# Kernel optimization log

Measured on AMD Instinct MI355X. Metric: run time of the kernel, lower is better.

Reference implementation:

```python
import jax, jax.numpy as jnp
import numpy as np

N = 20000      # nodes
E = 320000     # edges (avg degree 16)
S = 2          # extra feature axis (mean-pooled before fc)
IN = 128       # in_feats
H = 246        # n_hidden (must be 246 to match fc = Linear(246, 1))


def setup_inputs() -> dict:
    key = jax.random.key(0)
    ks = jax.random.split(key, 8)
    feat = jax.random.normal(ks[0], (N, S, IN), jnp.float32)
    src = jax.random.randint(ks[1], (E,), 0, N, jnp.int32)
    dst = jax.random.randint(ks[2], (E,), 0, N, jnp.int32)
    glorot = lambda k, shp, fan: jax.random.normal(k, shp, jnp.float32) / np.sqrt(fan).astype(np.float32)
    return {
        "features": feat,
        "src": src,
        "dst": dst,
        "W0": glorot(ks[3], (IN, H), IN), "b0": jnp.zeros((H,), jnp.float32),
        "W1": glorot(ks[4], (H, H), H),   "b1": jnp.zeros((H,), jnp.float32),
        "W2": glorot(ks[5], (H, H), H),   "b2": jnp.zeros((H,), jnp.float32),
        "fc_w": glorot(ks[6], (H, 1), H), "fc_b": jnp.zeros((1,), jnp.float32),
    }


def reference(features, src, dst, W0, b0, W1, b1, W2, b2, fc_w, fc_b):
    # DGL GraphConv, norm='both': h' = act( D_in^{-1/2} A D_out^{-1/2} h W + b )
    ones = jnp.ones((src.shape[0],), jnp.float32)
    out_deg = jax.ops.segment_sum(ones, src, num_segments=N)
    in_deg = jax.ops.segment_sum(ones, dst, num_segments=N)
    norm_out = jax.lax.rsqrt(jnp.maximum(out_deg, 1.0))[:, None, None]  # [N,1,1]
    norm_in = jax.lax.rsqrt(jnp.maximum(in_deg, 1.0))[:, None, None]

    def graph_conv(h, W, b):
        h = h * norm_out                                      # [N,S,F] scale by src-side norm
        agg = jax.ops.segment_sum(h[src], dst, num_segments=N)  # gather->scatter-add over edges
        agg = agg * norm_in
        return jax.nn.relu(agg @ W + b)

    h = graph_conv(features.astype(jnp.float32), W0, b0)
    # dropout between layers is identity in eval mode
    h = graph_conv(h, W1, b1)
    h = graph_conv(h, W2, b2)
    return h.mean(axis=1) @ fc_w + fc_b  # [N,1]
```

## Files before the change

kernel.cpp:

```cpp
#include <hip/hip_runtime.h>
#include <hip/hip_fp16.h>

#define NN 20000
#define NE 320000
#define SS 2
#define FIN 128
#define FH 246
#define MPAD 40064

typedef _Float16 f16x8 __attribute__((ext_vector_type(8)));
typedef float f32x4 __attribute__((ext_vector_type(4)));

__global__ void degree_kernel(const int* __restrict__ src, const int* __restrict__ dst,
                              int* __restrict__ deg_out, int* __restrict__ deg_in) {
    int e = blockIdx.x * blockDim.x + threadIdx.x;
    if (e < NE) {
        atomicAdd(&deg_out[src[e]], 1);
        atomicAdd(&deg_in[dst[e]], 1);
    }
}

__global__ void alloc_kernel(const int* __restrict__ deg_out, const int* __restrict__ deg_in,
                             float* __restrict__ norm_out, float* __restrict__ norm_in,
                             int* __restrict__ row_start, int* __restrict__ cursor,
                             int* __restrict__ counter) {
    __shared__ int smem[256];
    __shared__ int base_s;
    int tid = threadIdx.x;
    int i = blockIdx.x * 256 + tid;
    int v  = (i < NN) ? deg_in[i] : 0;
    int vp = (v + 3) & ~3;
    smem[tid] = vp;
    __syncthreads();
    for (int off = 1; off < 256; off <<= 1) {
        int t = (tid >= off) ? smem[tid - off] : 0;
        __syncthreads();
        smem[tid] += t;
        __syncthreads();
    }
    int incl = smem[tid];
    if (tid == 0) base_s = atomicAdd(counter, smem[255]);
    __syncthreads();
    if (i < NN) {
        int excl = base_s + incl - vp;
        row_start[i] = excl;
        cursor[i]    = excl;
        norm_out[i] = rsqrtf(fmaxf((float)deg_out[i], 1.0f));
        norm_in[i]  = rsqrtf(fmaxf((float)v, 1.0f));
    }
}

__global__ void scatter_kernel(const int* __restrict__ src, const int* __restrict__ dst,
                               int* __restrict__ cursor, ushort* __restrict__ sorted_src) {
    int e = blockIdx.x * blockDim.x + threadIdx.x;
    if (e < NE) {
        int d = dst[e];
        int pos = atomicAdd(&cursor[d], 1);
        sorted_src[pos] = (ushort)src[e];
    }
}

__global__ void pad_fill(const int* __restrict__ row_start, const int* __restrict__ deg_in,
                         ushort* __restrict__ sorted_src) {
    int n = blockIdx.x * 256 + threadIdx.x;
    if (n < NN) {
        int d = deg_in[n];
        int beg = row_start[n] + d;
        int end = row_start[n] + ((d + 3) & ~3);
        for (int p = beg; p < end; ++p) sorted_src[p] = (ushort)NN;
    }
}

__global__ void convert_w_all(const float* __restrict__ W0, const float* __restrict__ W1,
                              const float* __restrict__ W2,
                              ushort* __restrict__ Wh0, ushort* __restrict__ Wl0,
                              ushort* __restrict__ Wh1, ushort* __restrict__ Wl1,
                              ushort* __restrict__ Wh2, ushort* __restrict__ Wl2) {
    int n = blockIdx.x, k = threadIdx.x;
    const float* W; ushort* Wh; ushort* Wl; int K;
    if (blockIdx.y == 0)      { W = W0; Wh = Wh0; Wl = Wl0; K = FIN; }
    else if (blockIdx.y == 1) { W = W1; Wh = Wh1; Wl = Wl1; K = FH; }
    else                      { W = W2; Wh = Wh2; Wl = Wl2; K = FH; }
    float v = (k < K && n < 246) ? W[k * 246 + n] : 0.f;
    _Float16 h = (_Float16)v;
    _Float16 l = (_Float16)(v - (float)h);
    int c16 = n >> 4, lr = n & 15, kt = k >> 5, quad = (k >> 3) & 3, j = k & 7;
    int off = ((c16 * 8 + kt) * 64 + quad * 16 + lr) * 8 + j;
    Wh[off] = *(ushort*)&h;
    Wl[off] = *(ushort*)&l;
}

__global__ void init_out(float* __restrict__ out, const float* __restrict__ fcb,
                         float* __restrict__ norm_out) {
    int i = blockIdx.x * 256 + threadIdx.x;
    if (i < NN) out[i] = fcb[0];
    if (i == 0) norm_out[NN] = 0.f;
}

__global__ void zero_pads(ushort* __restrict__ Ah, ushort* __restrict__ Al) {
    int i = blockIdx.x * 256 + threadIdx.x;
    if (i < 4096) {
        int kt = i >> 9, r = i & 511;
        int m = NN * SS + (r >> 3), j = r & 7;
        size_t o = ((size_t)kt * MPAD + m) * 8 + j;
        ((unsigned long long*)Ah)[o] = 0ull;
        ((unsigned long long*)Al)[o] = 0ull;
    }
}

template<int F4ROW, int NCH, bool NORM>
__global__ void aggregate4(const float* __restrict__ h,
                           const int* __restrict__ row_start,
                           const int* __restrict__ deg_in,
                           const ushort* __restrict__ sorted_src,
                           const float* __restrict__ norm_out,
                           const float* __restrict__ norm_in,
                           ushort* __restrict__ Ah, ushort* __restrict__ Al) {
    constexpr int IHALF = F4ROW / 2;
    int g  = threadIdx.x >> 4;
    int l  = threadIdx.x & 15;
    int cb = blockIdx.x & (NCH - 1);
    int nb = blockIdx.x / NCH;
    int n  = nb * 8 + g;
    if (n >= NN) return;
    int idx = cb * 16 + l;
    const float4* hv = (const float4*)h;
    int beg = row_start[n];
    int end = beg + ((deg_in[n] + 3) & ~3);
    float4 acc = {0.f, 0.f, 0.f, 0.f};
    ushort4 ss;
    if (beg < end) ss = *(const ushort4*)&sorted_src[beg];
    for (int i = beg; i < end; i += 4) {
        ushort4 cur = ss;
        if (i + 4 < end) ss = *(const ushort4*)&sorted_src[i + 4];
        int s0 = cur.x, s1 = cur.y, s2 = cur.z, s3 = cur.w;
        if (NORM) {
            float n0 = norm_out[s0], n1 = norm_out[s1];
            float n2 = norm_out[s2], n3 = norm_out[s3];
            float4 v0 = hv[(size_t)(s0 < NN ? s0 : NN - 1) * F4ROW + idx];
            float4 v1 = hv[(size_t)(s1 < NN ? s1 : NN - 1) * F4ROW + idx];
            float4 v2 = hv[(size_t)(s2 < NN ? s2 : NN - 1) * F4ROW + idx];
            float4 v3 = hv[(size_t)(s3 < NN ? s3 : NN - 1) * F4ROW + idx];
            acc.x += v0.x * n0 + v1.x * n1 + v2.x * n2 + v3.x * n3;
            acc.y += v0.y * n0 + v1.y * n1 + v2.y * n2 + v3.y * n3;
            acc.z += v0.z * n0 + v1.z * n1 + v2.z * n2 + v3.z * n3;
            acc.w += v0.w * n0 + v1.w * n1 + v2.w * n2 + v3.w * n3;
        } else {
            float4 v0 = hv[(size_t)s0 * F4ROW + idx];
            float4 v1 = hv[(size_t)s1 * F4ROW + idx];
            float4 v2 = hv[(size_t)s2 * F4ROW + idx];
            float4 v3 = hv[(size_t)s3 * F4ROW + idx];
            acc.x += v0.x + v1.x + v2.x + v3.x;
            acc.y += v0.y + v1.y + v2.y + v3.y;
            acc.z += v0.z + v1.z + v2.z + v3.z;
            acc.w += v0.w + v1.w + v2.w + v3.w;
        }
    }
    float ni = norm_in[n];
    float v[4] = {acc.x * ni, acc.y * ni, acc.z * ni, acc.w * ni};
    ushort hp[4], lp[4];
#pragma unroll
    for (int j = 0; j < 4; ++j) {
        _Float16 hh = (_Float16)v[j];
        _Float16 ll = (_Float16)(v[j] - (float)hh);
        hp[j] = *(ushort*)&hh;
        lp[j] = *(ushort*)&ll;
    }
    int s  = (idx >= IHALF);
    int ik = idx & (IHALF - 1);
    size_t o = ((size_t)(ik >> 3) * MPAD + n * 2 + s) * 8 + (ik & 7);
    unsigned long long hv64, lv64;
    __builtin_memcpy(&hv64, hp, 8);
    __builtin_memcpy(&lv64, lp, 8);
    __builtin_nontemporal_store(hv64, (unsigned long long*)Ah + o);
    __builtin_nontemporal_store(lv64, (unsigned long long*)Al + o);
}

template<int KP, bool FUSE>
__global__ __launch_bounds__(256, 1) void gemm_breg(const ushort* __restrict__ Ah,
                                                    const ushort* __restrict__ Al,
                                                    const ushort* __restrict__ Whp,
                                                    const ushort* __restrict__ Wlp,
                                                    const float* __restrict__ b,
                                                    void* __restrict__ outv,
                                                    const float* __restrict__ fcw,
                                                    const float* __restrict__ nrm) {
    constexpr int NT = KP / 32;
    int tid  = threadIdx.x;
    int m0   = blockIdx.x * 64;
    int n0   = blockIdx.y * 128;
    int wave = tid >> 6, lane = tid & 63;
    int lr = lane & 15, quad = lane >> 4;
    int wcol = wave * 32;
    int c0 = (n0 + wcol) >> 4;

    f16x8 bh[2][NT], bl[2][NT];
#pragma unroll
    for (int ni = 0; ni < 2; ++ni)
#pragma unroll
        for (int kt = 0; kt < NT; ++kt) {
            size_t o = ((size_t)((c0 + ni) * 8 + kt) * 64 + lane) * 8;
            bh[ni][kt] = *(const f16x8*)(Whp + o);
            bl[ni][kt] = *(const f16x8*)(Wlp + o);
        }

    f32x4 acc[4][2];
#pragma unroll
    for (int mi = 0; mi < 4; ++mi)
#pragma unroll
        for (int ni = 0; ni < 2; ++ni) acc[mi][ni] = {0.f, 0.f, 0.f, 0.f};

#pragma unroll
    for (int t0 = 0; t0 < NT; ++t0) {
        f16x8 ah[4], al[4];
#pragma unroll
        for (int mi = 0; mi < 4; ++mi) {
            size_t fh = ((size_t)t0 * MPAD + m0 + mi * 16 + lr) * 32 + quad * 8;
            ah[mi] = *(const f16x8*)(Ah + fh);
            al[mi] = *(const f16x8*)(Al + fh);
        }
#pragma unroll
        for (int mi = 0; mi < 4; ++mi)
#pragma unroll
            for (int ni = 0; ni < 2; ++ni) {
                acc[mi][ni] = __builtin_amdgcn_mfma_f32_16x16x32_f16(ah[mi], bh[ni][t0], acc[mi][ni], 0, 0, 0);
                acc[mi][ni] = __builtin_amdgcn_mfma_f32_16x16x32_f16(al[mi], bh[ni][t0], acc[mi][ni], 0, 0, 0);
                acc[mi][ni] = __builtin_amdgcn_mfma_f32_16x16x32_f16(ah[mi], bl[ni][t0], acc[mi][ni], 0, 0, 0);
            }
    }

    if (FUSE) {
        float* out = (float*)outv;
#pragma unroll
        for (int mi = 0; mi < 4; ++mi) {
#pragma unroll
            for (int i = 0; i < 4; ++i) {
                float p = 0.f;
#pragma unroll
                for (int ni = 0; ni < 2; ++ni) {
                    int c = n0 + wcol + ni * 16 + lr;
                    if (c < 246)
                        p += fmaxf(acc[mi][ni][i] + b[c], 0.f) * fcw[c];
                }
#pragma unroll
                for (int off = 8; off > 0; off >>= 1)
                    p += __shfl_down(p, off, 16);
                int m = m0 + mi * 16 + quad * 4 + i;
                if (lr == 0 && m < NN * SS)
                    atomicAdd(&out[m >> 1], 0.5f * p);
            }
        }
    } else {
        float* outF = (float*)outv;
#pragma unroll
        for (int ni = 0; ni < 2; ++ni) {
            int c = n0 + wcol + ni * 16 + lr;
            float bj = (c < 246) ? b[c] : 0.f;
#pragma unroll
            for (int mi = 0; mi < 4; ++mi)
#pragma unroll
                for (int i = 0; i < 4; ++i) {
                    int m = m0 + mi * 16 + quad * 4 + i;
                    if (m < NN * SS) {
                        float no = nrm[m >> 1];
                        outF[(size_t)m * 256 + c] = fmaxf(acc[mi][ni][i] + bj, 0.f) * no;
                    }
                }
        }
    }
}

extern "C" void kernel_launch(void* const* d_in, const int* in_sizes, int n_in,
                              void* d_out, int out_size, void* d_ws, size_t ws_size,
                              hipStream_t stream) {
    const float* feat = (const float*)d_in[0];
    const int*   src  = (const int*)d_in[1];
    const int*   dst  = (const int*)d_in[2];
    const float* W0   = (const float*)d_in[3];
    const float* b0   = (const float*)d_in[4];
    const float* W1   = (const float*)d_in[5];
    const float* b1   = (const float*)d_in[6];
    const float* W2   = (const float*)d_in[7];
    const float* b2   = (const float*)d_in[8];
    const float* fcw  = (const float*)d_in[9];
    const float* fcb  = (const float*)d_in[10];
    float* out = (float*)d_out;

    char* ws = (char*)d_ws;
    size_t off = 0;
    auto alloc = [&](size_t bytes) {
        void* p = ws + off;
        off = (off + bytes + 255) & ~(size_t)255;
        return p;
    };
    int*    deg_out_i = (int*)alloc((2 * NN + 64) * sizeof(int));
    int*    deg_in_i  = deg_out_i + NN;
    int*    counter   = deg_out_i + 2 * NN;
    int*    row_start = (int*)alloc(NN * sizeof(int));
    int*    cursor    = (int*)alloc(NN * sizeof(int));
    ushort* sorted    = (ushort*)alloc((NE + 3 * NN + 16) * sizeof(ushort));
    float*  norm_out  = (float*)alloc((NN + 1) * sizeof(float));
    float*  norm_in   = (float*)alloc(NN * sizeof(float));
    ushort* Wh0 = (ushort*)alloc(256 * 256 * sizeof(ushort));
    ushort* Wl0 = (ushort*)alloc(256 * 256 * sizeof(ushort));
    ushort* Wh1 = (ushort*)alloc(256 * 256 * sizeof(ushort));
    ushort* Wl1 = (ushort*)alloc(256 * 256 * sizeof(ushort));
    ushort* Wh2 = (ushort*)alloc(256 * 256 * sizeof(ushort));
    ushort* Wl2 = (ushort*)alloc(256 * 256 * sizeof(ushort));
    ushort* Ahb = (ushort*)alloc((size_t)MPAD * 256 * sizeof(ushort));
    ushort* Alb = (ushort*)alloc((size_t)MPAD * 256 * sizeof(ushort));
    float*  bufH = (float*)alloc(((size_t)NN * SS * 256 + 512) * sizeof(float));

    hipMemsetAsync(deg_out_i, 0, (2 * NN + 1) * sizeof(int), stream);
    hipMemsetAsync(bufH + (size_t)NN * 512, 0, 512 * sizeof(float), stream);

    degree_kernel<<<(NE + 255) / 256, 256, 0, stream>>>(src, dst, deg_out_i, deg_in_i);
    alloc_kernel<<<(NN + 255) / 256, 256, 0, stream>>>(deg_out_i, deg_in_i, norm_out, norm_in,
                                                       row_start, cursor, counter);
    pad_fill<<<(NN + 255) / 256, 256, 0, stream>>>(row_start, deg_in_i, sorted);
    scatter_kernel<<<(NE + 255) / 256, 256, 0, stream>>>(src, dst, cursor, sorted);

    convert_w_all<<<dim3(256, 3), 256, 0, stream>>>(W0, W1, W2, Wh0, Wl0, Wh1, Wl1, Wh2, Wl2);
    init_out<<<(NN + 255) / 256, 256, 0, stream>>>(out, fcb, norm_out);
    zero_pads<<<16, 256, 0, stream>>>(Ahb, Alb);

    const int NB8 = (NN + 7) / 8;
    dim3 ggrid(MPAD / 64, 2);

    aggregate4<64, 4, true><<<NB8 * 4, 128, 0, stream>>>(feat, row_start, deg_in_i, sorted,
                                                         norm_out, norm_in, Ahb, Alb);
    gemm_breg<FIN, false><<<ggrid, 256, 0, stream>>>(Ahb, Alb, Wh0, Wl0, b0, bufH, fcw, norm_out);

    aggregate4<128, 8, false><<<NB8 * 8, 128, 0, stream>>>(bufH, row_start, deg_in_i, sorted,
                                                           norm_out, norm_in, Ahb, Alb);
    gemm_breg<256, false><<<ggrid, 256, 0, stream>>>(Ahb, Alb, Wh1, Wl1, b1, bufH, fcw, norm_out);

    aggregate4<128, 8, false><<<NB8 * 8, 128, 0, stream>>>(bufH, row_start, deg_in_i, sorted,
                                                           norm_out, norm_in, Ahb, Alb);
    gemm_breg<256, true><<<ggrid, 256, 0, stream>>>(Ahb, Alb, Wh2, Wl2, b2, out, fcw, norm_out);
}
```

Measured before the change: 388.7 us.

## Restructure GEMM into 2x2 wave tiling with double-buffered register prefetch

Replaces the GEMM that held all B fragments in registers with a 2x2 wave layout (each wave covers 32 rows by 64 cols). A and B fragments are now double-buffered per K step so the next tile's loads overlap the current MFMAs. Launch bounds are raised to allow 2 blocks per CU, and the aggregate kernel's nontemporal stores become plain stores. Reloading B every K step adds global or L2 traffic in exchange for fewer registers and higher occupancy.

```diff
diff --git a/kernel.cpp b/kernel.cpp
--- a/kernel.cpp
+++ b/kernel.cpp
@@ -169,15 +169,36 @@
     int s  = (idx >= IHALF);
     int ik = idx & (IHALF - 1);
     size_t o = ((size_t)(ik >> 3) * MPAD + n * 2 + s) * 8 + (ik & 7);
-    unsigned long long hv64, lv64;
-    __builtin_memcpy(&hv64, hp, 8);
-    __builtin_memcpy(&lv64, lp, 8);
-    __builtin_nontemporal_store(hv64, (unsigned long long*)Ah + o);
-    __builtin_nontemporal_store(lv64, (unsigned long long*)Al + o);
-}
+    ((unsigned long long*)Ah)[o] = *(unsigned long long*)hp;
+    ((unsigned long long*)Al)[o] = *(unsigned long long*)lp;
+}
+
+#define LOAD_A(T, AH, AL)                                                        \
+    _Pragma("unroll")                                                            \
+    for (int mi = 0; mi < 2; ++mi) {                                             \
+        size_t fh = ((size_t)(T) * MPAD + m0 + wm * 32 + mi * 16 + lr) * 32 + quad * 8; \
+        AH[mi] = *(const f16x8*)(Ah + fh);                                       \
+        AL[mi] = *(const f16x8*)(Al + fh);                                       \
+    }
+#define LOAD_B(T, BH, BL)                                                        \
+    _Pragma("unroll")                                                            \
+    for (int ni = 0; ni < 4; ++ni) {                                             \
+        size_t o = ((size_t)((c0 + ni) * 8 + (T)) * 64 + lane) * 8;              \
+        BH[ni] = *(const f16x8*)(Whp + o);                                       \
+        BL[ni] = *(const f16x8*)(Wlp + o);                                       \
+    }
+#define DO_MFMA(AH, AL, BH, BL)                                                  \
+    _Pragma("unroll")                                                            \
+    for (int mi = 0; mi < 2; ++mi)                                               \
+        _Pragma("unroll")                                                        \
+        for (int ni = 0; ni < 4; ++ni) {                                         \
+            acc[mi][ni] = __builtin_amdgcn_mfma_f32_16x16x32_f16(AH[mi], BH[ni], acc[mi][ni], 0, 0, 0); \
+            acc[mi][ni] = __builtin_amdgcn_mfma_f32_16x16x32_f16(AL[mi], BH[ni], acc[mi][ni], 0, 0, 0); \
+            acc[mi][ni] = __builtin_amdgcn_mfma_f32_16x16x32_f16(AH[mi], BL[ni], acc[mi][ni], 0, 0, 0); \
+        }
 
 template<int KP, bool FUSE>
-__global__ __launch_bounds__(256, 1) void gemm_breg(const ushort* __restrict__ Ah,
+__global__ __launch_bounds__(256, 2) void gemm_pipe(const ushort* __restrict__ Ah,
                                                     const ushort* __restrict__ Al,
                                                     const ushort* __restrict__ Whp,
                                                     const ushort* __restrict__ Wlp,
@@ -190,62 +211,48 @@
     int m0   = blockIdx.x * 64;
     int n0   = blockIdx.y * 128;
     int wave = tid >> 6, lane = tid & 63;
+    int wm = wave >> 1, wn = wave & 1;
     int lr = lane & 15, quad = lane >> 4;
-    int wcol = wave * 32;
-    int c0 = (n0 + wcol) >> 4;
-
-    f16x8 bh[2][NT], bl[2][NT];
-#pragma unroll
-    for (int ni = 0; ni < 2; ++ni)
-#pragma unroll
-        for (int kt = 0; kt < NT; ++kt) {
-            size_t o = ((size_t)((c0 + ni) * 8 + kt) * 64 + lane) * 8;
-            bh[ni][kt] = *(const f16x8*)(Whp + o);
-            bl[ni][kt] = *(const f16x8*)(Wlp + o);
-        }
-
-    f32x4 acc[4][2];
-#pragma unroll
-    for (int mi = 0; mi < 4; ++mi)
-#pragma unroll
-        for (int ni = 0; ni < 2; ++ni) acc[mi][ni] = {0.f, 0.f, 0.f, 0.f};
-
-#pragma unroll
-    for (int t0 = 0; t0 < NT; ++t0) {
-        f16x8 ah[4], al[4];
-#pragma unroll
-        for (int mi = 0; mi < 4; ++mi) {
-            size_t fh = ((size_t)t0 * MPAD + m0 + mi * 16 + lr) * 32 + quad * 8;
-            ah[mi] = *(const f16x8*)(Ah + fh);
-            al[mi] = *(const f16x8*)(Al + fh);
-        }
-#pragma unroll
-        for (int mi = 0; mi < 4; ++mi)
-#pragma unroll
-            for (int ni = 0; ni < 2; ++ni) {
-                acc[mi][ni] = __builtin_amdgcn_mfma_f32_16x16x32_f16(ah[mi], bh[ni][t0], acc[mi][ni], 0, 0, 0);
-                acc[mi][ni] = __builtin_amdgcn_mfma_f32_16x16x32_f16(al[mi], bh[ni][t0], acc[mi][ni], 0, 0, 0);
-                acc[mi][ni] = __builtin_amdgcn_mfma_f32_16x16x32_f16(ah[mi], bl[ni][t0], acc[mi][ni], 0, 0, 0);
-            }
+    int c0 = (n0 + wn * 64) >> 4;
+
+    f32x4 acc[2][4];
+#pragma unroll
+    for (int mi = 0; mi < 2; ++mi)
+#pragma unroll
+        for (int ni = 0; ni < 4; ++ni) acc[mi][ni] = {0.f, 0.f, 0.f, 0.f};
+
+    f16x8 a0h[2], a0l[2], b0h[4], b0l[4];
+    f16x8 a1h[2], a1l[2], b1h[4], b1l[4];
+    LOAD_A(0, a0h, a0l)
+    LOAD_B(0, b0h, b0l)
+#pragma unroll
+    for (int t = 0; t < NT; ++t) {
+        if (t & 1) {
+            if (t + 1 < NT) { LOAD_A(t + 1, a0h, a0l) LOAD_B(t + 1, b0h, b0l) }
+            DO_MFMA(a1h, a1l, b1h, b1l)
+        } else {
+            if (t + 1 < NT) { LOAD_A(t + 1, a1h, a1l) LOAD_B(t + 1, b1h, b1l) }
+            DO_MFMA(a0h, a0l, b0h, b0l)
+        }
     }
 
     if (FUSE) {
         float* out = (float*)outv;
 #pragma unroll
-        for (int mi = 0; mi < 4; ++mi) {
+        for (int mi = 0; mi < 2; ++mi) {
 #pragma unroll
             for (int i = 0; i < 4; ++i) {
                 float p = 0.f;
 #pragma unroll
-                for (int ni = 0; ni < 2; ++ni) {
-                    int c = n0 + wcol + ni * 16 + lr;
+                for (int ni = 0; ni < 4; ++ni) {
+                    int c = n0 + wn * 64 + ni * 16 + lr;
                     if (c < 246)
                         p += fmaxf(acc[mi][ni][i] + b[c], 0.f) * fcw[c];
                 }
 #pragma unroll
                 for (int off = 8; off > 0; off >>= 1)
                     p += __shfl_down(p, off, 16);
-                int m = m0 + mi * 16 + quad * 4 + i;
+                int m = m0 + wm * 32 + mi * 16 + quad * 4 + i;
                 if (lr == 0 && m < NN * SS)
                     atomicAdd(&out[m >> 1], 0.5f * p);
             }
@@ -253,14 +260,14 @@
     } else {
         float* outF = (float*)outv;
 #pragma unroll
-        for (int ni = 0; ni < 2; ++ni) {
-            int c = n0 + wcol + ni * 16 + lr;
+        for (int ni = 0; ni < 4; ++ni) {
+            int c = n0 + wn * 64 + ni * 16 + lr;
             float bj = (c < 246) ? b[c] : 0.f;
 #pragma unroll
-            for (int mi = 0; mi < 4; ++mi)
+            for (int mi = 0; mi < 2; ++mi)
 #pragma unroll
                 for (int i = 0; i < 4; ++i) {
-                    int m = m0 + mi * 16 + quad * 4 + i;
+                    int m = m0 + wm * 32 + mi * 16 + quad * 4 + i;
                     if (m < NN * SS) {
                         float no = nrm[m >> 1];
                         outF[(size_t)m * 256 + c] = fmaxf(acc[mi][ni][i] + bj, 0.f) * no;
@@ -329,13 +336,13 @@
 
     aggregate4<64, 4, true><<<NB8 * 4, 128, 0, stream>>>(feat, row_start, deg_in_i, sorted,
                                                          norm_out, norm_in, Ahb, Alb);
-    gemm_breg<FIN, false><<<ggrid, 256, 0, stream>>>(Ahb, Alb, Wh0, Wl0, b0, bufH, fcw, norm_out);
+    gemm_pipe<FIN, false><<<ggrid, 256, 0, stream>>>(Ahb, Alb, Wh0, Wl0, b0, bufH, fcw, norm_out);
 
     aggregate4<128, 8, false><<<NB8 * 8, 128, 0, stream>>>(bufH, row_start, deg_in_i, sorted,
                                                            norm_out, norm_in, Ahb, Alb);
-    gemm_breg<256, false><<<ggrid, 256, 0, stream>>>(Ahb, Alb, Wh1, Wl1, b1, bufH, fcw, norm_out);
+    gemm_pipe<256, false><<<ggrid, 256, 0, stream>>>(Ahb, Alb, Wh1, Wl1, b1, bufH, fcw, norm_out);
 
     aggregate4<128, 8, false><<<NB8 * 8, 128, 0, stream>>>(bufH, row_start, deg_in_i, sorted,
                                                            norm_out, norm_in, Ahb, Alb);
-    gemm_breg<256, true><<<ggrid, 256, 0, stream>>>(Ahb, Alb, Wh2, Wl2, b2, out, fcw, norm_out);
-}
+    gemm_pipe<256, true><<<ggrid, 256, 0, stream>>>(Ahb, Alb, Wh2, Wl2, b2, out, fcw, norm_out);
+}
```

New measurement: 353.8 us. 9.0% less time.

## Restructure GEMM to hold A rows in registers and stream weight tiles

Applied to the files above, without the earlier changes.

The GEMM kernel now runs one wave per block over 32 rows and keeps the full-K A fragments (high and low halves) in registers. It loops over all eight 32-column output chunks, loading weight fragments per chunk, where before each 256-thread block held a slice of W in registers and streamed A. For the fused last layer, the fc dot product is accumulated across all columns in registers, so only one atomic per row is issued instead of one per column block. The aggregate output stores also switch from nontemporal to ordinary stores. The trade-off is more weight traffic through cache and high register pressure from the large A arrays in exchange for reading A only once and fewer atomics.

```diff
diff --git a/kernel.cpp b/kernel.cpp
--- a/kernel.cpp
+++ b/kernel.cpp
@@ -169,104 +169,120 @@
     int s  = (idx >= IHALF);
     int ik = idx & (IHALF - 1);
     size_t o = ((size_t)(ik >> 3) * MPAD + n * 2 + s) * 8 + (ik & 7);
-    unsigned long long hv64, lv64;
-    __builtin_memcpy(&hv64, hp, 8);
-    __builtin_memcpy(&lv64, lp, 8);
-    __builtin_nontemporal_store(hv64, (unsigned long long*)Ah + o);
-    __builtin_nontemporal_store(lv64, (unsigned long long*)Al + o);
+    ((unsigned long long*)Ah)[o] = *(unsigned long long*)hp;
+    ((unsigned long long*)Al)[o] = *(unsigned long long*)lp;
 }
 
 template<int KP, bool FUSE>
-__global__ __launch_bounds__(256, 1) void gemm_breg(const ushort* __restrict__ Ah,
-                                                    const ushort* __restrict__ Al,
-                                                    const ushort* __restrict__ Whp,
-                                                    const ushort* __restrict__ Wlp,
-                                                    const float* __restrict__ b,
-                                                    void* __restrict__ outv,
-                                                    const float* __restrict__ fcw,
-                                                    const float* __restrict__ nrm) {
+__global__ __launch_bounds__(64) void gemm_rega(const ushort* __restrict__ Ah,
+                                                const ushort* __restrict__ Al,
+                                                const ushort* __restrict__ Whp,
+                                                const ushort* __restrict__ Wlp,
+                                                const float* __restrict__ b,
+                                                void* __restrict__ outv,
+                                                const float* __restrict__ fcw,
+                                                const float* __restrict__ nrm) {
     constexpr int NT = KP / 32;
-    int tid  = threadIdx.x;
-    int m0   = blockIdx.x * 64;
-    int n0   = blockIdx.y * 128;
-    int wave = tid >> 6, lane = tid & 63;
+    int lane = threadIdx.x;
+    int m0   = blockIdx.x * 32;
     int lr = lane & 15, quad = lane >> 4;
-    int wcol = wave * 32;
-    int c0 = (n0 + wcol) >> 4;
-
-    f16x8 bh[2][NT], bl[2][NT];
-#pragma unroll
-    for (int ni = 0; ni < 2; ++ni)
+
+    f16x8 ah[2][NT], al[2][NT];
+#pragma unroll
+    for (int mi = 0; mi < 2; ++mi)
 #pragma unroll
         for (int kt = 0; kt < NT; ++kt) {
-            size_t o = ((size_t)((c0 + ni) * 8 + kt) * 64 + lane) * 8;
-            bh[ni][kt] = *(const f16x8*)(Whp + o);
-            bl[ni][kt] = *(const f16x8*)(Wlp + o);
-        }
-
-    f32x4 acc[4][2];
-#pragma unroll
-    for (int mi = 0; mi < 4; ++mi)
-#pragma unroll
-        for (int ni = 0; ni < 2; ++ni) acc[mi][ni] = {0.f, 0.f, 0.f, 0.f};
-
-#pragma unroll
-    for (int t0 = 0; t0 < NT; ++t0) {
-        f16x8 ah[4], al[4];
-#pragma unroll
-        for (int mi = 0; mi < 4; ++mi) {
-            size_t fh = ((size_t)t0 * MPAD + m0 + mi * 16 + lr) * 32 + quad * 8;
-            ah[mi] = *(const f16x8*)(Ah + fh);
-            al[mi] = *(const f16x8*)(Al + fh);
-        }
-#pragma unroll
-        for (int mi = 0; mi < 4; ++mi)
+            size_t fh = ((size_t)kt * MPAD + m0 + mi * 16 + lr) * 32 + quad * 8;
+            ah[mi][kt] = *(const f16x8*)(Ah + fh);
+            al[mi][kt] = *(const f16x8*)(Al + fh);
+        }
+
+    float no[2][4];
+    int   mrow[2][4];
+#pragma unroll
+    for (int mi = 0; mi < 2; ++mi)
+#pragma unroll
+        for (int i = 0; i < 4; ++i) {
+            int m = m0 + mi * 16 + quad * 4 + i;
+            mrow[mi][i] = m;
+            no[mi][i] = (m < NN * SS) ? nrm[m >> 1] : 0.f;
+        }
+
+    float pacc[2][4];
+    if (FUSE) {
+#pragma unroll
+        for (int mi = 0; mi < 2; ++mi)
+#pragma unroll
+            for (int i = 0; i < 4; ++i) pacc[mi][i] = 0.f;
+    }
+
+    float* outF = (float*)outv;
+
+#pragma unroll
+    for (int nc = 0; nc < 8; ++nc) {
+        f32x4 acc[2][2];
+#pragma unroll
+        for (int mi = 0; mi < 2; ++mi)
+#pragma unroll
+            for (int ni = 0; ni < 2; ++ni) acc[mi][ni] = {0.f, 0.f, 0.f, 0.f};
+
+#pragma unroll
+        for (int t = 0; t < NT; ++t) {
+            f16x8 bh[2], bl[2];
 #pragma unroll
             for (int ni = 0; ni < 2; ++ni) {
-                acc[mi][ni] = __builtin_amdgcn_mfma_f32_16x16x32_f16(ah[mi], bh[ni][t0], acc[mi][ni], 0, 0, 0);
-                acc[mi][ni] = __builtin_amdgcn_mfma_f32_16x16x32_f16(al[mi], bh[ni][t0], acc[mi][ni], 0, 0, 0);
-                acc[mi][ni] = __builtin_amdgcn_mfma_f32_16x16x32_f16(ah[mi], bl[ni][t0], acc[mi][ni], 0, 0, 0);
+                size_t o = ((size_t)((nc * 2 + ni) * 8 + t) * 64 + lane) * 8;
+                bh[ni] = *(const f16x8*)(Whp + o);
+                bl[ni] = *(const f16x8*)(Wlp + o);
             }
+#pragma unroll
+            for (int mi = 0; mi < 2; ++mi)
+#pragma unroll
+                for (int ni = 0; ni < 2; ++ni) {
+                    acc[mi][ni] = __builtin_amdgcn_mfma_f32_16x16x32_f16(ah[mi][t], bh[ni], acc[mi][ni], 0, 0, 0);
+                    acc[mi][ni] = __builtin_amdgcn_mfma_f32_16x16x32_f16(al[mi][t], bh[ni], acc[mi][ni], 0, 0, 0);
+                    acc[mi][ni] = __builtin_amdgcn_mfma_f32_16x16x32_f16(ah[mi][t], bl[ni], acc[mi][ni], 0, 0, 0);
+                }
+        }
+
+#pragma unroll
+        for (int ni = 0; ni < 2; ++ni) {
+            int c = nc * 32 + ni * 16 + lr;
+            float bj = (c < 246) ? b[c] : 0.f;
+            if (FUSE) {
+                float fw = (c < 246) ? fcw[c] : 0.f;
+#pragma unroll
+                for (int mi = 0; mi < 2; ++mi)
+#pragma unroll
+                    for (int i = 0; i < 4; ++i)
+                        pacc[mi][i] += fmaxf(acc[mi][ni][i] + bj, 0.f) * fw;
+            } else {
+#pragma unroll
+                for (int mi = 0; mi < 2; ++mi)
+#pragma unroll
+                    for (int i = 0; i < 4; ++i) {
+                        int m = mrow[mi][i];
+                        if (m < NN * SS)
+                            outF[(size_t)m * 256 + c] = fmaxf(acc[mi][ni][i] + bj, 0.f) * no[mi][i];
+                    }
+            }
+        }
     }
 
     if (FUSE) {
         float* out = (float*)outv;
 #pragma unroll
-        for (int mi = 0; mi < 4; ++mi) {
+        for (int mi = 0; mi < 2; ++mi)
 #pragma unroll
             for (int i = 0; i < 4; ++i) {
-                float p = 0.f;
-#pragma unroll
-                for (int ni = 0; ni < 2; ++ni) {
-                    int c = n0 + wcol + ni * 16 + lr;
-                    if (c < 246)
-                        p += fmaxf(acc[mi][ni][i] + b[c], 0.f) * fcw[c];
-                }
+                float p = pacc[mi][i];
 #pragma unroll
                 for (int off = 8; off > 0; off >>= 1)
                     p += __shfl_down(p, off, 16);
-                int m = m0 + mi * 16 + quad * 4 + i;
+                int m = mrow[mi][i];
                 if (lr == 0 && m < NN * SS)
                     atomicAdd(&out[m >> 1], 0.5f * p);
             }
-        }
-    } else {
-        float* outF = (float*)outv;
-#pragma unroll
-        for (int ni = 0; ni < 2; ++ni) {
-            int c = n0 + wcol + ni * 16 + lr;
-            float bj = (c < 246) ? b[c] : 0.f;
-#pragma unroll
-            for (int mi = 0; mi < 4; ++mi)
-#pragma unroll
-                for (int i = 0; i < 4; ++i) {
-                    int m = m0 + mi * 16 + quad * 4 + i;
-                    if (m < NN * SS) {
-                        float no = nrm[m >> 1];
-                        outF[(size_t)m * 256 + c] = fmaxf(acc[mi][ni][i] + bj, 0.f) * no;
-                    }
-                }
-        }
     }
 }
 
@@ -325,17 +341,17 @@
     zero_pads<<<16, 256, 0, stream>>>(Ahb, Alb);
 
     const int NB8 = (NN + 7) / 8;
-    dim3 ggrid(MPAD / 64, 2);
+    const int GG  = MPAD / 32;
 
     aggregate4<64, 4, true><<<NB8 * 4, 128, 0, stream>>>(feat, row_start, deg_in_i, sorted,
                                                          norm_out, norm_in, Ahb, Alb);
-    gemm_breg<FIN, false><<<ggrid, 256, 0, stream>>>(Ahb, Alb, Wh0, Wl0, b0, bufH, fcw, norm_out);
+    gemm_rega<FIN, false><<<GG, 64, 0, stream>>>(Ahb, Alb, Wh0, Wl0, b0, bufH, fcw, norm_out);
 
     aggregate4<128, 8, false><<<NB8 * 8, 128, 0, stream>>>(bufH, row_start, deg_in_i, sorted,
                                                            norm_out, norm_in, Ahb, Alb);
-    gemm_breg<256, false><<<ggrid, 256, 0, stream>>>(Ahb, Alb, Wh1, Wl1, b1, bufH, fcw, norm_out);
+    gemm_rega<256, false><<<GG, 64, 0, stream>>>(Ahb, Alb, Wh1, Wl1, b1, bufH, fcw, norm_out);
 
     aggregate4<128, 8, false><<<NB8 * 8, 128, 0, stream>>>(bufH, row_start, deg_in_i, sorted,
                                                            norm_out, norm_in, Ahb, Alb);
-    gemm_breg<256, true><<<ggrid, 256, 0, stream>>>(Ahb, Alb, Wh2, Wl2, b2, out, fcw, norm_out);
-}
+    gemm_rega<256, true><<<GG, 64, 0, stream>>>(Ahb, Alb, Wh2, Wl2, b2, out, fcw, norm_out);
+}
```

Measured after the change: 398.5 us. 2.5% more time.
